# Kernel optimization log

Hardware: AMD Instinct MI355X
Metric: run time of the kernel (lower is better)

The kernel has to match this reference:

```python
import jax, jax.numpy as jnp
import numpy as np


def _lga_pass(x, filters, radius):
    # x: [N, C, H, W]; filters: [N, (2r+1)^2, H, W]
    # out[n,c,h,w] = sum_{i,j in [-r,r]} filters[n,(i+r)*(2r+1)+(j+r),h,w] * x[n,c,h+i,w+j]
    N, C, H, W = x.shape
    k = 2 * radius + 1
    xp = jnp.pad(x, ((0, 0), (0, 0), (radius, radius), (radius, radius)))
    out = jnp.zeros_like(x)
    idx = 0
    for i in range(k):  # fixed small kernel loop (25 taps), accumulates without materializing [N,C,H,W,25]
        for j in range(k):
            out = out + filters[:, idx:idx + 1] * xp[:, :, i:i + H, j:j + W]
            idx += 1
    return out


def setup_inputs() -> dict:
    key = jax.random.key(0)
    k1, k2 = jax.random.split(key)
    input1 = jax.random.normal(k1, (2, 64, 256, 512), dtype=jnp.float32)
    input2 = jax.random.uniform(k2, (2, 25, 256, 512), dtype=jnp.float32)
    return {"input1": input1, "input2": input2, "radius": 2}


def reference(input1, input2, radius):
    # LGA applied twice with the same per-pixel filters (Lga2Function.forward)
    temp = _lga_pass(input1, input2, radius)
    out = _lga_pass(temp, input2, radius)
    return out
```

## Files before the change

kernel.cpp:

```cpp
#include <hip/hip_runtime.h>
#include <hip/hip_fp16.h>


typedef __fp16 h2v __attribute__((ext_vector_type(2)));

#define OH 12
#define OW 60
#define USH 76

__device__ __forceinline__ unsigned pkh(float a, float b) {
    union { h2v h; unsigned u; } c;
    c.h = __builtin_amdgcn_cvt_pkrtz(a, b);
    return c.u;
}

#define PKFL(ac, fv, xv) \
    asm("v_pk_fma_f16 %0, %1, %2, %0 op_sel:[0,0,0] op_sel_hi:[0,1,1]" \
        : "+v"(ac) : "v"(fv), "v"(xv));
#define PKFH(ac, fv, xv) \
    asm("v_pk_fma_f16 %0, %1, %2, %0 op_sel:[1,0,0] op_sel_hi:[1,1,1]" \
        : "+v"(ac) : "v"(fv), "v"(xv));

#define ROW8(T, qa, qb, A0, A1, A2, A3) \
  PKFL(A0, frA[T+0], qa.x) PKFH(A1, frA[T+0], qa.y) PKFL(A2, frB[T+0], qa.z) PKFH(A3, frB[T+0], qa.w) \
  PKFL(A0, frA[T+1], qa.y) PKFH(A1, frA[T+1], qa.z) PKFL(A2, frB[T+1], qa.w) PKFH(A3, frB[T+1], qb.x) \
  PKFL(A0, frA[T+2], qa.z) PKFH(A1, frA[T+2], qa.w) PKFL(A2, frB[T+2], qb.x) PKFH(A3, frB[T+2], qb.y) \
  PKFL(A0, frA[T+3], qa.w) PKFH(A1, frA[T+3], qb.x) PKFL(A2, frB[T+3], qb.y) PKFH(A3, frB[T+3], qb.z) \
  PKFL(A0, frA[T+4], qb.x) PKFH(A1, frA[T+4], qb.y) PKFL(A2, frB[T+4], qb.z) PKFH(A3, frB[T+4], qb.w)

#define PASS2(BUF, ROWBASE, S0, S1, S2, S3) { \
    unsigned e0=0u,e1=0u,e2=0u,e3=0u,o0=0u,o1=0u,o2=0u,o3=0u; \
    _Pragma("unroll") \
    for (int i = 0; i < 5; ++i) { \
        const int b = ((ROWBASE) + i) * USH + 4 * s; \
        uint4 qa = *(const uint4*)&(BUF)[b]; \
        uint4 qb = *(const uint4*)&(BUF)[b + 4]; \
        if (i & 1) { ROW8(5*i, qa, qb, o0, o1, o2, o3) } \
        else       { ROW8(5*i, qa, qb, e0, e1, e2, e3) } \
    } \
    asm("v_pk_add_f16 %0, %1, %2" : "=v"(S0) : "v"(e0), "v"(o0)); \
    asm("v_pk_add_f16 %0, %1, %2" : "=v"(S1) : "v"(e1), "v"(o1)); \
    asm("v_pk_add_f16 %0, %1, %2" : "=v"(S2) : "v"(e2), "v"(o2)); \
    asm("v_pk_add_f16 %0, %1, %2" : "=v"(S3) : "v"(e3), "v"(o3)); }

#define LBAR() { asm volatile("s_waitcnt lgkmcnt(0)" ::: "memory"); \
                 __builtin_amdgcn_s_barrier(); asm volatile("" ::: "memory"); }

__global__ __launch_bounds__(256)
void lga2_fused(const float* __restrict__ x, const float* __restrict__ f,
                float* __restrict__ out, int N, int C, int H, int W, int CPB) {
    const int tid = threadIdx.x;
    const int r = tid >> 4;
    const int s = tid & 15;
    const int oh0 = blockIdx.y * OH;
    const int ow0 = blockIdx.x * OW;
    const int CG = C / CPB;
    const int n  = blockIdx.z / CG;
    const int c0 = (blockIdx.z % CG) * CPB;
    const int HW = H * W;

    __shared__ unsigned sxU[2][20 * USH];
    __shared__ unsigned stU[16 * USH];

    if (tid < 64) {
        int row = tid >> 2, q = tid & 3;
        stU[row * USH + (q < 2 ? q : q + 64)] = 0u;
    }

    const int gh_f = oh0 - 2 + r;
    const int gwb  = ow0 - 2 + 4 * s;
    const bool rowok = (gh_f >= 0) && (gh_f < H);
    const bool p0ok = rowok && (gwb >= 0) && (gwb + 1 < W);
    const bool p1ok = rowok && (gwb + 3 < W);
    const float* fb = f + (size_t)(n * 25) * HW + (size_t)(rowok ? gh_f : 0) * W;

    unsigned frA[25], frB[25];
    #pragma unroll
    for (int t = 0; t < 25; ++t) {
        float2 v01 = p0ok ? *(const float2*)(fb + (size_t)t * HW + gwb)
                          : make_float2(0.f, 0.f);
        float2 v23 = p1ok ? *(const float2*)(fb + (size_t)t * HW + gwb + 2)
                          : make_float2(0.f, 0.f);
        frA[t] = pkh(v01.x, v01.y);
        frB[t] = pkh(v23.x, v23.y);
        if (t == 12) __builtin_amdgcn_sched_barrier(0);
    }
    #pragma unroll
    for (int t = 0; t < 25; ++t)
        asm volatile("" : "+v"(frA[t]), "+v"(frB[t]));

    const int i1 = tid + 256;
    const bool has1 = (tid < 340 - 256);
    const int row0 = tid / 17, v0 = tid - row0 * 17;
    const int row1 = i1 / 17,  v1 = i1 - row1 * 17;
    const int g0h = oh0 - 4 + row0, g0c = ow0 - 4 + 4 * v0;
    const int g1h = oh0 - 4 + row1, g1c = ow0 - 4 + 4 * v1;
    const bool ok0 = (g0h >= 0) && (g0h < H) && (g0c >= 0) && (g0c + 3 < W);
    const bool ok1 = has1 && (g1h >= 0) && (g1h < H) && (g1c >= 0) && (g1c + 3 < W);
    const int off0 = ok0 ? (g0h * W + g0c) : 0;
    const int off1 = ok1 ? (g1h * W + g1c) : 0;
    const int l0u = row0 * USH + 4 * v0;
    const int l1u = row1 * USH + 4 * v1;

    const float4 z4 = make_float4(0.f, 0.f, 0.f, 0.f);
    const float* xc = x + (size_t)(n * C + c0) * HW;

#define PACK4(pa, pb) make_uint4(pkh(pa.x, pb.x), pkh(pa.y, pb.y), \
                                 pkh(pa.z, pb.z), pkh(pa.w, pb.w))

    {
        float4 pa = ok0 ? *(const float4*)(xc + off0) : z4;
        float4 pb = ok0 ? *(const float4*)(xc + HW + off0) : z4;
        *(uint4*)&sxU[0][l0u] = PACK4(pa, pb);
        if (has1) {
            float4 qa = ok1 ? *(const float4*)(xc + off1) : z4;
            float4 qb = ok1 ? *(const float4*)(xc + HW + off1) : z4;
            *(uint4*)&sxU[0][l1u] = PACK4(qa, qb);
        }
    }
    __syncthreads();

    const bool prow = (r >= 2) && (r <= 13) && (gh_f < H);
    const int rc = (r < 2) ? 2 : ((r > 13) ? 13 : r);
    float* op = out + ((size_t)(n * C + c0) * H + gh_f) * W + gwb;

    int cur = 0;
    for (int cp = 0; cp < CPB; cp += 2) {
        float4 n0a = z4, n0b = z4, n1a = z4, n1b = z4;
        const bool pf = (cp + 2 < CPB);
        if (pf) {
            const float* xn = xc + (size_t)(cp + 2) * HW;
            if (ok0) { n0a = *(const float4*)(xn + off0);
                       n0b = *(const float4*)(xn + HW + off0); }
            if (ok1) { n1a = *(const float4*)(xn + off1);
                       n1b = *(const float4*)(xn + HW + off1); }
        }

        unsigned t0, t1, t2, t3;
        PASS2(sxU[cur], r, t0, t1, t2, t3)
        *(uint2*)&stU[r * USH + 2 + 4 * s] = make_uint2(t0, t1);
        *(uint2*)&stU[r * USH + 4 + 4 * s] = make_uint2(t2, t3);
        LBAR();

        PASS2(stU, rc - 2, t0, t1, t2, t3)
        if (prow) {
            union { unsigned u; h2v h; } U0, U1, U2, U3;
            U0.u = t0; U1.u = t1; U2.u = t2; U3.u = t3;
            float* oq = op + HW;
            if (s >= 1 && gwb + 1 < W) {
                *(float2*)op = make_float2((float)U0.h.x, (float)U1.h.x);
                *(float2*)oq = make_float2((float)U0.h.y, (float)U1.h.y);
            }
            if (s <= 14 && gwb + 3 < W) {
                *(float2*)(op + 2) = make_float2((float)U2.h.x, (float)U3.h.x);
                *(float2*)(oq + 2) = make_float2((float)U2.h.y, (float)U3.h.y);
            }
        }

        if (pf) {
            unsigned* d = sxU[cur ^ 1];
            *(uint4*)&d[l0u] = PACK4(n0a, n0b);
            if (has1) *(uint4*)&d[l1u] = PACK4(n1a, n1b);
        }
        LBAR();
        cur ^= 1;
        op += 2 * (size_t)HW;
    }
}

extern "C" void kernel_launch(void* const* d_in, const int* in_sizes, int n_in,
                              void* d_out, int out_size, void* d_ws, size_t ws_size,
                              hipStream_t stream) {
    const float* x = (const float*)d_in[0];
    const float* f = (const float*)d_in[1];
    float* out = (float*)d_out;

    const int N = 2, C = 64, H = 256, W = 512;
    const int CPB = 32;
    const int CG = C / CPB;

    dim3 grid((W + OW - 1) / OW,
              (H + OH - 1) / OH,
              N * CG);
    lga2_fused<<<grid, 256, 0, stream>>>(x, f, out, N, C, H, W, CPB);
}
```

Before: 69.67 us.

## Process four channels per iteration with quad-buffered shared tiles

Restructures the channel loop so each iteration handles two channel pairs (four channels) with four x shared buffers and two intermediate buffers. This halves the number of barriers per channel and interleaves two independent PASS2 chains for more ILP. Global prefetch loads are split, with one pair issued before the first pass and the other between passes, to overlap memory latency with compute. It raises LDS usage and register pressure, which may reduce occupancy.

```diff
diff --git a/kernel.cpp b/kernel.cpp
--- a/kernel.cpp
+++ b/kernel.cpp
@@ -45,6 +45,64 @@
 
 #define LBAR() { asm volatile("s_waitcnt lgkmcnt(0)" ::: "memory"); \
                  __builtin_amdgcn_s_barrier(); asm volatile("" ::: "memory"); }
+
+#define PACK4(pa, pb) make_uint4(pkh(pa.x, pb.x), pkh(pa.y, pb.y), \
+                                 pkh(pa.z, pb.z), pkh(pa.w, pb.w))
+
+#define STORES(P, S0, S1, S2, S3) { \
+    union { unsigned u; h2v h; } U0, U1, U2, U3; \
+    U0.u = S0; U1.u = S1; U2.u = S2; U3.u = S3; \
+    float* oq_ = (P) + HW; \
+    if (s >= 1 && gwb + 1 < W) { \
+        *(float2*)(P)  = make_float2((float)U0.h.x, (float)U1.h.x); \
+        *(float2*)oq_  = make_float2((float)U0.h.y, (float)U1.h.y); \
+    } \
+    if (s <= 14 && gwb + 3 < W) { \
+        *(float2*)((P) + 2) = make_float2((float)U2.h.x, (float)U3.h.x); \
+        *(float2*)(oq_ + 2) = make_float2((float)U2.h.y, (float)U3.h.y); \
+    } }
+
+#define QBODY(CB, Ra, Rb, La, Lb) { \
+    float4 a0a=z4, a0b=z4, a1a=z4, a1b=z4; \
+    const bool pfA = (CB) + 4 < CPB; \
+    if (pfA) { \
+        if (ok0) { a0a = *(const float4*)pfp0; a0b = *(const float4*)(pfp0 + HW); } \
+        if (ok1) { a1a = *(const float4*)pfp1; a1b = *(const float4*)(pfp1 + HW); } \
+    } \
+    unsigned t0, t1, t2, t3, u0, u1, u2, u3; \
+    PASS2(Ra, r, t0, t1, t2, t3) \
+    PASS2(Rb, r, u0, u1, u2, u3) \
+    *(uint2*)&stA[r * USH + 2 + 4 * s] = make_uint2(t0, t1); \
+    *(uint2*)&stA[r * USH + 4 + 4 * s] = make_uint2(t2, t3); \
+    *(uint2*)&stB[r * USH + 2 + 4 * s] = make_uint2(u0, u1); \
+    *(uint2*)&stB[r * USH + 4 + 4 * s] = make_uint2(u2, u3); \
+    LBAR(); \
+    if (pfA) { \
+        *(uint4*)&(La)[l0u] = PACK4(a0a, a0b); \
+        if (has1) *(uint4*)&(La)[l1u] = PACK4(a1a, a1b); \
+    } \
+    float4 b0a=z4, b0b=z4, b1a=z4, b1b=z4; \
+    const bool pfB = (CB) + 6 < CPB; \
+    if (pfB) { \
+        if (ok0) { b0a = *(const float4*)(pfp0 + 2 * (size_t)HW); \
+                   b0b = *(const float4*)(pfp0 + 3 * (size_t)HW); } \
+        if (ok1) { b1a = *(const float4*)(pfp1 + 2 * (size_t)HW); \
+                   b1b = *(const float4*)(pfp1 + 3 * (size_t)HW); } \
+    } \
+    PASS2(stA, rc - 2, t0, t1, t2, t3) \
+    PASS2(stB, rc - 2, u0, u1, u2, u3) \
+    if (prow) { \
+        STORES(op, t0, t1, t2, t3) \
+        STORES(op + 2 * (size_t)HW, u0, u1, u2, u3) \
+    } \
+    if (pfB) { \
+        *(uint4*)&(Lb)[l0u] = PACK4(b0a, b0b); \
+        if (has1) *(uint4*)&(Lb)[l1u] = PACK4(b1a, b1b); \
+    } \
+    LBAR(); \
+    pfp0 += 4 * (size_t)HW; pfp1 += 4 * (size_t)HW; \
+    op += 4 * (size_t)HW; \
+}
 
 __global__ __launch_bounds__(256)
 void lga2_fused(const float* __restrict__ x, const float* __restrict__ f,
@@ -59,12 +117,14 @@
     const int c0 = (blockIdx.z % CG) * CPB;
     const int HW = H * W;
 
-    __shared__ unsigned sxU[2][20 * USH];
-    __shared__ unsigned stU[16 * USH];
-
-    if (tid < 64) {
-        int row = tid >> 2, q = tid & 3;
-        stU[row * USH + (q < 2 ? q : q + 64)] = 0u;
+    __shared__ unsigned sxA[20 * USH], sxB[20 * USH];
+    __shared__ unsigned sxC[20 * USH], sxD[20 * USH];
+    __shared__ unsigned stA[16 * USH], stB[16 * USH];
+
+    if (tid < 128) {
+        unsigned* stz = (tid < 64) ? stA : stB;
+        int i = tid & 63, row = i >> 2, q = i & 3;
+        stz[row * USH + (q < 2 ? q : q + 64)] = 0u;
     }
 
     const int gh_f = oh0 - 2 + r;
@@ -105,17 +165,20 @@
     const float4 z4 = make_float4(0.f, 0.f, 0.f, 0.f);
     const float* xc = x + (size_t)(n * C + c0) * HW;
 
-#define PACK4(pa, pb) make_uint4(pkh(pa.x, pb.x), pkh(pa.y, pb.y), \
-                                 pkh(pa.z, pb.z), pkh(pa.w, pb.w))
-
     {
         float4 pa = ok0 ? *(const float4*)(xc + off0) : z4;
         float4 pb = ok0 ? *(const float4*)(xc + HW + off0) : z4;
-        *(uint4*)&sxU[0][l0u] = PACK4(pa, pb);
+        *(uint4*)&sxA[l0u] = PACK4(pa, pb);
+        float4 pc = ok0 ? *(const float4*)(xc + 2 * (size_t)HW + off0) : z4;
+        float4 pd = ok0 ? *(const float4*)(xc + 3 * (size_t)HW + off0) : z4;
+        *(uint4*)&sxB[l0u] = PACK4(pc, pd);
         if (has1) {
             float4 qa = ok1 ? *(const float4*)(xc + off1) : z4;
             float4 qb = ok1 ? *(const float4*)(xc + HW + off1) : z4;
-            *(uint4*)&sxU[0][l1u] = PACK4(qa, qb);
+            *(uint4*)&sxA[l1u] = PACK4(qa, qb);
+            float4 qc = ok1 ? *(const float4*)(xc + 2 * (size_t)HW + off1) : z4;
+            float4 qd = ok1 ? *(const float4*)(xc + 3 * (size_t)HW + off1) : z4;
+            *(uint4*)&sxB[l1u] = PACK4(qc, qd);
         }
     }
     __syncthreads();
@@ -123,48 +186,12 @@
     const bool prow = (r >= 2) && (r <= 13) && (gh_f < H);
     const int rc = (r < 2) ? 2 : ((r > 13) ? 13 : r);
     float* op = out + ((size_t)(n * C + c0) * H + gh_f) * W + gwb;
-
-    int cur = 0;
-    for (int cp = 0; cp < CPB; cp += 2) {
-        float4 n0a = z4, n0b = z4, n1a = z4, n1b = z4;
-        const bool pf = (cp + 2 < CPB);
-        if (pf) {
-            const float* xn = xc + (size_t)(cp + 2) * HW;
-            if (ok0) { n0a = *(const float4*)(xn + off0);
-                       n0b = *(const float4*)(xn + HW + off0); }
-            if (ok1) { n1a = *(const float4*)(xn + off1);
-                       n1b = *(const float4*)(xn + HW + off1); }
-        }
-
-        unsigned t0, t1, t2, t3;
-        PASS2(sxU[cur], r, t0, t1, t2, t3)
-        *(uint2*)&stU[r * USH + 2 + 4 * s] = make_uint2(t0, t1);
-        *(uint2*)&stU[r * USH + 4 + 4 * s] = make_uint2(t2, t3);
-        LBAR();
-
-        PASS2(stU, rc - 2, t0, t1, t2, t3)
-        if (prow) {
-            union { unsigned u; h2v h; } U0, U1, U2, U3;
-            U0.u = t0; U1.u = t1; U2.u = t2; U3.u = t3;
-            float* oq = op + HW;
-            if (s >= 1 && gwb + 1 < W) {
-                *(float2*)op = make_float2((float)U0.h.x, (float)U1.h.x);
-                *(float2*)oq = make_float2((float)U0.h.y, (float)U1.h.y);
-            }
-            if (s <= 14 && gwb + 3 < W) {
-                *(float2*)(op + 2) = make_float2((float)U2.h.x, (float)U3.h.x);
-                *(float2*)(oq + 2) = make_float2((float)U2.h.y, (float)U3.h.y);
-            }
-        }
-
-        if (pf) {
-            unsigned* d = sxU[cur ^ 1];
-            *(uint4*)&d[l0u] = PACK4(n0a, n0b);
-            if (has1) *(uint4*)&d[l1u] = PACK4(n1a, n1b);
-        }
-        LBAR();
-        cur ^= 1;
-        op += 2 * (size_t)HW;
+    const float* pfp0 = xc + 4 * (size_t)HW + off0;
+    const float* pfp1 = xc + 4 * (size_t)HW + off1;
+
+    for (int cq = 0; cq < CPB; cq += 8) {
+        QBODY(cq,     sxA, sxB, sxC, sxD)
+        QBODY(cq + 4, sxC, sxD, sxA, sxB)
     }
 }
 
```

Measured after the change: 68.59 us, median of 2. Within noise of the previous version (-1.6%).
